# Optimization experiments

Measured on AMD Instinct MI355X. Metric: run time of the kernel, lower is better.

## Reference

```python
import jax, jax.numpy as jnp
import numpy as np

NODE_DIM = 2
EMB_DIM = 128
SEQ_LEN = 201  # must be odd: depot + N pickups + N deliveries
BATCH = 2048


def _basesin(x, T, fai=0.0):
    return np.sin(2 * np.pi / T * np.abs(np.mod(x, 2 * T) - T) + fai)


def _basecos(x, T, fai=0.0):
    return np.cos(2 * np.pi / T * np.abs(np.mod(x, 2 * T) - T) + fai)


def cyclic_position_encoding_pattern(n_position, emb_dim, mean_pooling=True):
    Td_set = np.linspace(np.power(n_position, 1 / (emb_dim // 2)), n_position,
                         emb_dim // 2, dtype='int')
    x = np.zeros((n_position, emb_dim))
    for i in range(emb_dim):
        Td = Td_set[i // 3 * 3 + 1] if i // 3 * 3 + 1 < emb_dim // 2 else Td_set[-1]
        fai = 0 if i <= emb_dim // 2 else 2 * np.pi * ((-i + emb_dim // 2) / (emb_dim // 2))
        longer = np.arange(0, np.ceil(n_position / Td) * Td, 0.01)
        sel = np.linspace(0, len(longer), n_position, dtype='int', endpoint=False)
        if i % 2 == 1:
            x[:, i] = _basecos(longer, Td, fai)[sel]
        else:
            x[:, i] = _basesin(longer, Td, fai)[sel]
    pattern = x.astype(np.float32)
    pattern_sum = np.zeros_like(pattern)
    arange = np.arange(n_position)
    pooling = [-2, -1, 0, 1, 2] if mean_pooling else [0]
    for i in pooling:
        pattern_sum += pattern[(arange + i + n_position) % n_position]
    pattern = pattern_sum / len(pooling) - pattern.mean(0, keepdims=True)
    return jnp.asarray(pattern)


def setup_inputs() -> dict:
    key = jax.random.key(0)
    kx, kw = jax.random.split(key)
    x = jax.random.normal(kx, (BATCH, SEQ_LEN, NODE_DIM), dtype=jnp.float32)
    # random cyclic permutation per batch: cycle visits all nodes starting at 0
    rng = np.random.default_rng(0)
    r = rng.random((BATCH, SEQ_LEN - 1))
    order = np.concatenate([np.zeros((BATCH, 1), dtype=np.int64),
                            np.argsort(r, axis=1).astype(np.int64) + 1], axis=1)
    nxt = np.roll(order, -1, axis=1)
    sol = np.zeros((BATCH, SEQ_LEN), dtype=np.int64)
    np.put_along_axis(sol, order, nxt, axis=1)
    solutions = jnp.asarray(sol)
    # Linear(node_dim, emb_dim, bias=False), init uniform(-stdv, stdv), stdv=1/sqrt(in)
    stdv = 1.0 / np.sqrt(NODE_DIM)
    W = jax.random.uniform(kw, (EMB_DIM, NODE_DIM), dtype=jnp.float32,
                           minval=-stdv, maxval=stdv)
    pattern = cyclic_position_encoding_pattern(SEQ_LEN, EMB_DIM)
    return {"x": x, "solutions": solutions, "W": W, "pattern": pattern}


def _position_indices(solutions):
    """Pointer-chase over the solution cycle; returns visited_time [B,S] int32
    and top2 [B,S,2] int32 (clac_stacks=True path of the original)."""
    B, S = solutions.shape
    half = S // 2
    arange = jnp.arange(B)
    sol = solutions.astype(jnp.int32)

    visited0 = jnp.zeros((B, S), dtype=jnp.int32)
    pre0 = jnp.zeros((B,), dtype=jnp.int32)
    stacks0 = jnp.full((B, half + 1), -0.01, dtype=jnp.float32).at[:, 0].set(0.0)
    top20 = jnp.zeros((B, S, 2), dtype=jnp.int32)

    def step(carry, i):
        visited, pre, stacks, top2 = carry
        cur = sol[arange, pre]                       # [B] current node
        visited = visited.at[arange, cur].set(i + 1)
        # pickups (0 < cur <= half) push i+1; deliveries (cur > half) pop (-0.01);
        # depot (cur == 0) is a no-op (rewrites stacks[:,0] with itself).
        pos = jnp.where(cur > half, cur - half, cur)
        val = jnp.where(cur == 0, stacks[arange, 0],
                        jnp.where(cur > half, jnp.float32(-0.01),
                                  (i + 1).astype(jnp.float32)))
        stacks = stacks.at[arange, pos].set(val)
        _, idx = jax.lax.top_k(stacks, 2)            # [B,2]
        top2 = top2.at[arange, cur].set(idx.astype(jnp.int32))
        return (visited, cur, stacks, top2), None

    (visited, _, _, top2), _ = jax.lax.scan(
        step, (visited0, pre0, stacks0, top20), jnp.arange(S))
    return visited, top2


def reference(x, solutions, W, pattern):
    visited_time, top2 = _position_indices(solutions)
    S = solutions.shape[1]
    # pos_enc[b, j] = pattern[visited_time[b, j] % S]
    pos_enc = jnp.take(pattern, visited_time % S, axis=0)   # [B,S,D]
    x_embedding = jnp.einsum('bsn,dn->bsd', x, W)           # Linear, no bias
    return x_embedding, pos_enc, visited_time.astype(jnp.int64), top2
```

## Files before the change

kernel.cpp:

```cpp
#include <hip/hip_runtime.h>
#include <stdint.h>

#define B 2048
#define S 201
#define HALF 100
#define D 128
#define BS (B * S)
#define OFF_POS (BS * D)
#define OFF_VT  (2 * OFF_POS)
#define OFF_T2  (OFF_VT + BS)
#define EMB_F4  (BS * (D / 4))

#define NCH 32
#define NEMB 2016
#define NB1 (NCH + NEMB)
#define TPB 256

typedef float  vf4 __attribute__((ext_vector_type(4)));
typedef float  vf2 __attribute__((ext_vector_type(2)));

__global__ __launch_bounds__(TPB) void k1(const float* __restrict__ x,
                                          const int* __restrict__ sol,
                                          const float* __restrict__ W,
                                          float* __restrict__ out,
                                          uint8_t* __restrict__ vt_ws) {
    if (blockIdx.x < NCH) {
        __shared__ uint8_t  s_sol[64 * S];
        __shared__ uint8_t  s_nx [64 * (HALF+1)];
        __shared__ uint8_t  s_pv [64 * (HALF+1)];
        __shared__ uint8_t  s_vis[64 * S];
        __shared__ uint16_t s_t2 [64 * S];
        const int tid = threadIdx.x;
        const int b0  = blockIdx.x * 64;

        for (int idx = tid; idx < 64 * S; idx += TPB) {
            s_sol[idx] = (uint8_t)sol[b0 * S + idx];
            s_vis[idx] = 0;
            s_t2[idx]  = 0;
        }
        __syncthreads();

        if (tid < 64) {
            uint8_t*  sl  = s_sol + tid * S;
            uint8_t*  nx  = s_nx  + tid * (HALF + 1);
            uint8_t*  pv  = s_pv  + tid * (HALF + 1);
            uint8_t*  vis = s_vis + tid * S;
            uint16_t* t2  = s_t2  + tid * S;

            int pre = 0;
            int head = 0, second = 1;
            unsigned long long m0 = 0, m1 = 0;

            for (int i = 0; i < S; ++i) {
                int cur = sl[pre];
                vis[cur] = (uint8_t)(i + 1);
                if (cur != 0) {
                    if (cur <= HALF) {
                        nx[cur]  = (uint8_t)head;
                        pv[head] = (uint8_t)cur;
                        second = head;
                        head   = cur;
                        if (cur < 64) m0 |= 1ull << cur; else m1 |= 1ull << (cur - 64);
                    } else {
                        int q = cur - HALF;
                        bool in = (q < 64) ? ((m0 >> q) & 1ull) : ((m1 >> (q - 64)) & 1ull);
                        if (in) {
                            if (q < 64) m0 &= ~(1ull << q); else m1 &= ~(1ull << (q - 64));
                            if (q == head) {
                                head = second;
                                second = (head == 0) ? 1 : (int)nx[head];
                            } else if (q == second) {
                                int n2 = nx[q];
                                nx[head] = (uint8_t)n2;
                                pv[n2]   = (uint8_t)head;
                                second = n2;
                            } else {
                                int p = pv[q], n2 = nx[q];
                                nx[p]  = (uint8_t)n2;
                                pv[n2] = (uint8_t)p;
                            }
                        }
                    }
                }
                t2[cur] = (uint16_t)(head | (second << 8));
                pre = cur;
            }
        }
        __syncthreads();

        for (int idx = tid; idx < 64 * S; idx += TPB) {
            int v = s_vis[idx];
            out[OFF_VT + b0 * S + idx] = (float)v;
            vt_ws[b0 * S + idx] = (uint8_t)v;
            int t = s_t2[idx];
            vf2 f2 = { (float)(t & 255), (float)(t >> 8) };
            __builtin_nontemporal_store(f2, ((vf2*)(out + OFF_T2)) + b0 * S + idx);
        }
    } else {
        const int d4 = (int)(threadIdx.x & 31);
        const float4* W4 = (const float4*)W;
        float4 w0 = W4[d4 * 2];
        float4 w1 = W4[d4 * 2 + 1];
        const float2* x2 = (const float2*)x;
        vf4* o4 = (vf4*)out;
        const int stride = NEMB * TPB;
        for (int idx4 = (int)(blockIdx.x - NCH) * TPB + (int)threadIdx.x;
             idx4 < EMB_F4; idx4 += stride) {
            float2 xv = x2[idx4 >> 5];
            vf4 o;
            o.x = xv.x * w0.x + xv.y * w0.y;
            o.y = xv.x * w0.z + xv.y * w0.w;
            o.z = xv.x * w1.x + xv.y * w1.y;
            o.w = xv.x * w1.z + xv.y * w1.w;
            __builtin_nontemporal_store(o, &o4[idx4]);
        }
    }
}

__global__ __launch_bounds__(TPB) void k2(const float* __restrict__ pattern,
                                          const uint8_t* __restrict__ vt_ws,
                                          float* __restrict__ out) {
    const vf4* p4 = (const vf4*)pattern;
    vf4* o4 = (vf4*)(out + OFF_POS);
    const int stride = (int)(gridDim.x * blockDim.x);
    for (int idx4 = (int)(blockIdx.x * blockDim.x + threadIdx.x);
         idx4 < EMB_F4; idx4 += stride) {
        int vt = vt_ws[idx4 >> 5];
        int row = (vt >= S) ? (vt - S) : vt;
        vf4 v = p4[row * 32 + (idx4 & 31)];
        __builtin_nontemporal_store(v, &o4[idx4]);
    }
}

extern "C" void kernel_launch(void* const* d_in, const int* in_sizes, int n_in,
                              void* d_out, int out_size, void* d_ws, size_t ws_size,
                              hipStream_t stream) {
    const float* x       = (const float*)d_in[0];
    const int*   sol     = (const int*)d_in[1];
    const float* W       = (const float*)d_in[2];
    const float* pattern = (const float*)d_in[3];
    float* out = (float*)d_out;
    uint8_t* vt_ws = (uint8_t*)d_ws;

    hipLaunchKernelGGL(k1, dim3(NB1), dim3(TPB), 0, stream, x, sol, W, out, vt_ws);
    hipLaunchKernelGGL(k2, dim3(2048), dim3(TPB), 0, stream, pattern, vt_ws, out);
}
```

Measured before the change: 466.7 us.

## Fuse sequential scan, embedding and positional gather into one per-batch kernel

Replaces the two-kernel design with one block per batch element. Wave 0 runs the serial stack scan (one thread) while the other three waves compute the linear embedding. After a block barrier, all threads gather pattern rows into pos_enc using visit times held in shared memory. This removes the workspace round-trip and the second launch, and overlaps the serial scan with embedding writes. The cost is that each serial scan now occupies only one lane, so overall scan parallelism depends on how many blocks can be resident at once.

```diff
diff --git a/kernel.cpp b/kernel.cpp
--- a/kernel.cpp
+++ b/kernel.cpp
@@ -9,103 +9,84 @@
 #define OFF_POS (BS * D)
 #define OFF_VT  (2 * OFF_POS)
 #define OFF_T2  (OFF_VT + BS)
-#define EMB_F4  (BS * (D / 4))
-
-#define NCH 32
-#define NEMB 2016
-#define NB1 (NCH + NEMB)
+#define F4B (S * (D / 4))
 #define TPB 256
 
-typedef float  vf4 __attribute__((ext_vector_type(4)));
-typedef float  vf2 __attribute__((ext_vector_type(2)));
+typedef float vf4 __attribute__((ext_vector_type(4)));
+typedef float vf2 __attribute__((ext_vector_type(2)));
 
-__global__ __launch_bounds__(TPB) void k1(const float* __restrict__ x,
-                                          const int* __restrict__ sol,
-                                          const float* __restrict__ W,
-                                          float* __restrict__ out,
-                                          uint8_t* __restrict__ vt_ws) {
-    if (blockIdx.x < NCH) {
-        __shared__ uint8_t  s_sol[64 * S];
-        __shared__ uint8_t  s_nx [64 * (HALF+1)];
-        __shared__ uint8_t  s_pv [64 * (HALF+1)];
-        __shared__ uint8_t  s_vis[64 * S];
-        __shared__ uint16_t s_t2 [64 * S];
-        const int tid = threadIdx.x;
-        const int b0  = blockIdx.x * 64;
+__global__ __launch_bounds__(TPB, 4) void fused(const float* __restrict__ x,
+                                                const int* __restrict__ sol,
+                                                const float* __restrict__ W,
+                                                const float* __restrict__ pattern,
+                                                float* __restrict__ out) {
+    __shared__ uint8_t  s_sol[S];
+    __shared__ uint8_t  s_vis[S];
+    __shared__ uint8_t  s_nx[HALF + 1];
+    __shared__ uint8_t  s_pv[HALF + 1];
+    __shared__ uint16_t s_t2[S];
 
-        for (int idx = tid; idx < 64 * S; idx += TPB) {
-            s_sol[idx] = (uint8_t)sol[b0 * S + idx];
-            s_vis[idx] = 0;
-            s_t2[idx]  = 0;
+    const int tid = threadIdx.x;
+    const int b   = blockIdx.x;
+
+    if (tid < 64) {
+        for (int j = tid; j < S; j += 64) {
+            s_sol[j] = (uint8_t)sol[b * S + j];
+            s_vis[j] = 0;
+            s_t2[j]  = 0;
         }
-        __syncthreads();
+        asm volatile("s_waitcnt lgkmcnt(0)" ::: "memory");
 
-        if (tid < 64) {
-            uint8_t*  sl  = s_sol + tid * S;
-            uint8_t*  nx  = s_nx  + tid * (HALF + 1);
-            uint8_t*  pv  = s_pv  + tid * (HALF + 1);
-            uint8_t*  vis = s_vis + tid * S;
-            uint16_t* t2  = s_t2  + tid * S;
-
+        if (tid == 0) {
             int pre = 0;
             int head = 0, second = 1;
             unsigned long long m0 = 0, m1 = 0;
 
             for (int i = 0; i < S; ++i) {
-                int cur = sl[pre];
-                vis[cur] = (uint8_t)(i + 1);
+                int cur = s_sol[pre];
+                s_vis[cur] = (uint8_t)(i + 1);
                 if (cur != 0) {
                     if (cur <= HALF) {
-                        nx[cur]  = (uint8_t)head;
-                        pv[head] = (uint8_t)cur;
+                        s_nx[cur]  = (uint8_t)head;
+                        s_pv[head] = (uint8_t)cur;
                         second = head;
                         head   = cur;
                         if (cur < 64) m0 |= 1ull << cur; else m1 |= 1ull << (cur - 64);
                     } else {
                         int q = cur - HALF;
-                        bool in = (q < 64) ? ((m0 >> q) & 1ull) : ((m1 >> (q - 64)) & 1ull);
+                        bool in = (q < 64) ? ((m0 >> q) & 1ull)
+                                           : ((m1 >> (q - 64)) & 1ull);
                         if (in) {
                             if (q < 64) m0 &= ~(1ull << q); else m1 &= ~(1ull << (q - 64));
                             if (q == head) {
                                 head = second;
-                                second = (head == 0) ? 1 : (int)nx[head];
+                                second = (head == 0) ? 1 : (int)s_nx[head];
                             } else if (q == second) {
-                                int n2 = nx[q];
-                                nx[head] = (uint8_t)n2;
-                                pv[n2]   = (uint8_t)head;
+                                int n2 = s_nx[q];
+                                s_nx[head] = (uint8_t)n2;
+                                s_pv[n2]   = (uint8_t)head;
                                 second = n2;
                             } else {
-                                int p = pv[q], n2 = nx[q];
-                                nx[p]  = (uint8_t)n2;
-                                pv[n2] = (uint8_t)p;
+                                int p = s_pv[q], n2 = s_nx[q];
+                                s_nx[p]  = (uint8_t)n2;
+                                s_pv[n2] = (uint8_t)p;
                             }
                         }
                     }
                 }
-                t2[cur] = (uint16_t)(head | (second << 8));
+                s_t2[cur] = (uint16_t)(head | (second << 8));
                 pre = cur;
             }
         }
-        __syncthreads();
-
-        for (int idx = tid; idx < 64 * S; idx += TPB) {
-            int v = s_vis[idx];
-            out[OFF_VT + b0 * S + idx] = (float)v;
-            vt_ws[b0 * S + idx] = (uint8_t)v;
-            int t = s_t2[idx];
-            vf2 f2 = { (float)(t & 255), (float)(t >> 8) };
-            __builtin_nontemporal_store(f2, ((vf2*)(out + OFF_T2)) + b0 * S + idx);
-        }
     } else {
-        const int d4 = (int)(threadIdx.x & 31);
+        const int t  = tid - 64;
+        const int d4 = t & 31;
         const float4* W4 = (const float4*)W;
         float4 w0 = W4[d4 * 2];
         float4 w1 = W4[d4 * 2 + 1];
-        const float2* x2 = (const float2*)x;
-        vf4* o4 = (vf4*)out;
-        const int stride = NEMB * TPB;
-        for (int idx4 = (int)(blockIdx.x - NCH) * TPB + (int)threadIdx.x;
-             idx4 < EMB_F4; idx4 += stride) {
+        const float2* x2 = (const float2*)x + b * S;
+        vf4* o4 = (vf4*)out + b * F4B;
+        for (int idx4 = t; idx4 < F4B; idx4 += 192) {
             float2 xv = x2[idx4 >> 5];
             vf4 o;
             o.x = xv.x * w0.x + xv.y * w0.y;
@@ -115,20 +96,23 @@
             __builtin_nontemporal_store(o, &o4[idx4]);
         }
     }
-}
+    __syncthreads();
 
-__global__ __launch_bounds__(TPB) void k2(const float* __restrict__ pattern,
-                                          const uint8_t* __restrict__ vt_ws,
-                                          float* __restrict__ out) {
-    const vf4* p4 = (const vf4*)pattern;
-    vf4* o4 = (vf4*)(out + OFF_POS);
-    const int stride = (int)(gridDim.x * blockDim.x);
-    for (int idx4 = (int)(blockIdx.x * blockDim.x + threadIdx.x);
-         idx4 < EMB_F4; idx4 += stride) {
-        int vt = vt_ws[idx4 >> 5];
-        int row = (vt >= S) ? (vt - S) : vt;
-        vf4 v = p4[row * 32 + (idx4 & 31)];
-        __builtin_nontemporal_store(v, &o4[idx4]);
+    {
+        const vf4* p4 = (const vf4*)pattern;
+        vf4* o4 = (vf4*)(out + OFF_POS) + b * F4B;
+        for (int idx4 = tid; idx4 < F4B; idx4 += TPB) {
+            int vt  = s_vis[idx4 >> 5];
+            int row = (vt >= S) ? (vt - S) : vt;
+            vf4 v = p4[row * 32 + (idx4 & 31)];
+            __builtin_nontemporal_store(v, &o4[idx4]);
+        }
+        for (int j = tid; j < S; j += TPB) {
+            out[OFF_VT + b * S + j] = (float)s_vis[j];
+            int tt = s_t2[j];
+            vf2 f2 = { (float)(tt & 255), (float)(tt >> 8) };
+            __builtin_nontemporal_store(f2, ((vf2*)(out + OFF_T2)) + b * S + j);
+        }
     }
 }
 
@@ -140,8 +124,6 @@
     const float* W       = (const float*)d_in[2];
     const float* pattern = (const float*)d_in[3];
     float* out = (float*)d_out;
-    uint8_t* vt_ws = (uint8_t*)d_ws;
 
-    hipLaunchKernelGGL(k1, dim3(NB1), dim3(TPB), 0, stream, x, sol, W, out, vt_ws);
-    hipLaunchKernelGGL(k2, dim3(2048), dim3(TPB), 0, stream, pattern, vt_ws, out);
+    hipLaunchKernelGGL(fused, dim3(B), dim3(TPB), 0, stream, x, sol, W, pattern, out);
 }
```

After: 430.4 us. 7.8% less time.
